# Performance work log

Hardware: AMD Instinct MI355X
Metric: run time of the kernel (lower is better)

Reference implementation:

```python
import jax, jax.numpy as jnp
import numpy as np

C = 3            # image_channels
X = 192          # cortex_x_count
Y = 192          # cortex_y_count
RF = 24          # receptive field height/width
IMG = 224        # input image H/W (must be >= max rf_start + RF)
EXK = 38         # excitatory lateral window (i-19:i+19)
INK = 94         # inhibitory lateral window (i-47:i+47)
PAD = 47         # activation padding used by the original module
GAMMA_E = 0.9
GAMMA_I = 0.9


def setup_inputs() -> dict:
    key = jax.random.key(0)
    ks = jax.random.split(key, 9)
    return {
        "input": jax.random.normal(ks[0], (C, IMG, IMG), jnp.float32),
        "afferent_weights": jax.random.normal(ks[1], (C, X, Y, RF, RF), jnp.float32),
        "ex_lateral_weight": jax.random.normal(ks[2], (EXK, EXK), jnp.float32),
        "in_lateral_weight": jax.random.normal(ks[3], (INK, INK), jnp.float32),
        "afferent_mask": jax.random.uniform(ks[4], (RF, RF), jnp.float32),
        "ex_lateral_mask": jax.random.uniform(ks[5], (EXK, EXK), jnp.float32),
        "in_lateral_mask": jax.random.uniform(ks[6], (INK, INK), jnp.float32),
        "old_activation": jax.random.normal(ks[7], (C, X, Y), jnp.float32),
        "cortex_rf_start": jax.random.randint(ks[8], (X, Y, 2), 0, IMG - RF + 1, jnp.int32),
    }


def _lateral(old_pad, kernel2d, out_start):
    # Depthwise correlation: same 2D kernel applied to every channel.
    # old_pad: (C, X+2*PAD, Y+2*PAD); treat channels as batch.
    y = jax.lax.conv_general_dilated(
        old_pad[:, None],              # (C, 1, Hp, Wp)
        kernel2d[None, None],          # (1, 1, K, K)
        window_strides=(1, 1),
        padding="VALID",
    )[:, 0]                            # (C, Ho, Wo)
    return y[:, out_start:out_start + X, out_start:out_start + Y]


def reference(input, afferent_weights, ex_lateral_weight, in_lateral_weight,
              afferent_mask, ex_lateral_mask, in_lateral_mask,
              old_activation, cortex_rf_start):
    # --- afferent: per-pixel locally-connected receptive fields ---
    u = jnp.arange(RF)
    ix = cortex_rf_start[..., 0][:, :, None, None] + u[None, None, :, None]  # (X,Y,RF,1)
    iy = cortex_rf_start[..., 1][:, :, None, None] + u[None, None, None, :]  # (X,Y,1,RF)
    patches = input[:, ix, iy]                                               # (C,X,Y,RF,RF)
    afferent = jnp.einsum("cxyuv,cxyuv->xy", patches,
                          afferent_weights * afferent_mask)                  # (X,Y)

    # --- lateral fields over padded previous activation ---
    old_pad = jnp.pad(old_activation, ((0, 0), (PAD, PAD), (PAD, PAD)))
    # excitatory window [i-19:i+19] centered at cell (i+47) -> start offset 28
    exc = _lateral(old_pad, ex_lateral_weight * ex_lateral_mask, PAD - 19)
    # inhibitory window [i-47:i+47] -> start offset 0
    inh = _lateral(old_pad, in_lateral_weight * in_lateral_mask, PAD - 47)

    # afferent sum is a scalar per cortex location, shared across channels
    return jnp.broadcast_to(afferent[None], (C, X, Y)) + GAMMA_E * exc - GAMMA_I * inh
```

## Files before the change

### kernel.cpp

```cpp
#include <hip/hip_runtime.h>

#define XD 192
#define YD 192
#define CCH 3
#define IMG 224

#define OFF_PAD 0
#define PADW 320
#define N_PAD (CCH*XD*PADW)
#define OFF_KI (OFF_PAD + N_PAD)
#define KI_LD 96
#define N_KI (94*KI_LD)
#define OFF_KE (OFF_KI + N_KI)
#define KE_LD 40
#define N_KE (38*KE_LD)

#define N_OUT (CCH*XD*YD)

#define QSPLIT 8
#define NCONV 576
#define NAFF 9216

typedef __attribute__((ext_vector_type(4))) float f32x4;

__global__ __launch_bounds__(256) void k_prep(
    const float* __restrict__ exw, const float* __restrict__ exm,
    const float* __restrict__ inw, const float* __restrict__ inm,
    const float* __restrict__ oldact, float* __restrict__ ws,
    float* __restrict__ out)
{
    const int TOT = N_OUT + N_PAD + N_KI + N_KE;
    for (int idx = blockIdx.x * 256 + threadIdx.x; idx < TOT; idx += gridDim.x * 256) {
        if (idx < N_OUT) {
            out[idx] = 0.f;
        } else if (idx < N_OUT + N_PAD) {
            const int k = idx - N_OUT;
            const int col = k % PADW;
            const int rem = k / PADW;
            float v = 0.f;
            if (col >= 64 && col < 64 + YD)
                v = oldact[rem * YD + (col - 64)];
            ws[OFF_PAD + k] = v;
        } else if (idx < N_OUT + N_PAD + N_KI) {
            const int k = idx - N_OUT - N_PAD;
            const int i = k / KI_LD, j = k % KI_LD;
            ws[OFF_KI + k] = (j < 94) ? (-0.9f * inw[i * 94 + j] * inm[i * 94 + j]) : 0.f;
        } else {
            const int k = idx - N_OUT - N_PAD - N_KI;
            const int i = k / KE_LD, j = k % KE_LD;
            ws[OFF_KE + k] = (j < 38) ? (0.9f * exw[i * 38 + j] * exm[i * 38 + j]) : 0.f;
        }
    }
}

__global__ __launch_bounds__(256, 3) void k_fused(
    const float* __restrict__ input, const float* __restrict__ affw,
    const float* __restrict__ affm, const int* __restrict__ rfstart,
    const float* __restrict__ ws, float* __restrict__ out)
{
    const int bid = blockIdx.x;
    const int tid = threadIdx.x;

    if (bid < NCONV) {
        const int xt = bid % 24;
        const int c  = (bid / 24) % 3;
        const int q  = bid / 72;
        const int yg = tid & 31;
        const int xr = tid >> 5;
        const int x  = xt * 8 + xr;
        const int y0 = yg * 6;

        float acc[6] = {0.f, 0.f, 0.f, 0.f, 0.f, 0.f};
        const float* pad = ws + OFF_PAD + (size_t)c * XD * PADW;

        for (int i = q; i < 94; i += QSPLIT) {
            const int r = x + i - 47;
            if (r < 0 || r >= XD) continue;
            const float* row = pad + r * PADW + y0 + 17;
            const float4* kw = (const float4*)(ws + OFF_KI + i * KI_LD);
            float w[9];
            #pragma unroll
            for (int k = 0; k < 9; ++k) w[k] = row[k];
            #pragma unroll
            for (int g = 0; g < 24; ++g) {
                const float4 k4 = kw[g];
                #pragma unroll
                for (int t = 0; t < 6; ++t) {
                    acc[t] += k4.x * w[0 + t];
                    acc[t] += k4.y * w[1 + t];
                    acc[t] += k4.z * w[2 + t];
                    acc[t] += k4.w * w[3 + t];
                }
                #pragma unroll
                for (int k = 0; k < 5; ++k) w[k] = w[k + 4];
                #pragma unroll
                for (int k = 5; k < 9; ++k) w[k] = row[4 * (g + 1) + k];
            }
        }

        for (int i = q; i < 38; i += QSPLIT) {
            const int r = x + i - 19;
            if (r < 0 || r >= XD) continue;
            const float* row = pad + r * PADW + y0 + 45;
            const float4* kw = (const float4*)(ws + OFF_KE + i * KE_LD);
            float w[9];
            #pragma unroll
            for (int k = 0; k < 9; ++k) w[k] = row[k];
            #pragma unroll
            for (int g = 0; g < 10; ++g) {
                const float4 k4 = kw[g];
                #pragma unroll
                for (int t = 0; t < 6; ++t) {
                    acc[t] += k4.x * w[0 + t];
                    acc[t] += k4.y * w[1 + t];
                    acc[t] += k4.z * w[2 + t];
                    acc[t] += k4.w * w[3 + t];
                }
                #pragma unroll
                for (int k = 0; k < 5; ++k) w[k] = w[k + 4];
                #pragma unroll
                for (int k = 5; k < 9; ++k) w[k] = row[4 * (g + 1) + k];
            }
        }

        float* op = out + ((size_t)c * XD + x) * YD + y0;
        #pragma unroll
        for (int t = 0; t < 6; ++t) atomicAdd(&op[t], acc[t]);

    } else {
        const int wv_id = __builtin_amdgcn_readfirstlane(tid >> 6);
        const int xy    = (bid - NCONV) * 4 + wv_id;
        const int lane  = tid & 63;
        const int sx = rfstart[xy * 2 + 0];
        const int sy = rfstart[xy * 2 + 1];
        const f32x4* W4 = (const f32x4*)affw + (size_t)xy * 144;
        const f32x4* M4 = (const f32x4*)affm;

        f32x4 wv[7], mv[7], iv[7];

        #pragma unroll
        for (int it = 0; it < 7; ++it) {
            const int g0 = lane + (it << 6);
            const int g  = (g0 < 432) ? g0 : 0;
            const int c  = (g >= 288) ? 2 : ((g >= 144) ? 1 : 0);
            const int r  = g - c * 144;
            const f32x4* wp = W4 + (size_t)c * 5308416 + r;
            asm volatile("global_load_dwordx4 %0, %1, off"
                         : "=v"(wv[it]) : "v"(wp));
            const int u  = (r * 2731) >> 14;
            const int v  = (r - u * 6) << 2;
            const float* ip = input + c * (IMG * IMG) + (sx + u) * IMG + (sy + v);
            asm volatile("global_load_dwordx4 %0, %1, off"
                         : "=v"(iv[it]) : "v"(ip));
            const f32x4* mp = M4 + r;
            asm volatile("global_load_dwordx4 %0, %1, off"
                         : "=v"(mv[it]) : "v"(mp));
        }
        asm volatile("s_waitcnt vmcnt(0)" ::: "memory");
        __builtin_amdgcn_sched_barrier(0);

        float acc = 0.f;
        #pragma unroll
        for (int it = 0; it < 7; ++it) {
            const int g0 = lane + (it << 6);
            const float z = (g0 < 432) ? 1.f : 0.f;
            acc += iv[it].x * (z * mv[it].x) * wv[it].x;
            acc += iv[it].y * (z * mv[it].y) * wv[it].y;
            acc += iv[it].z * (z * mv[it].z) * wv[it].z;
            acc += iv[it].w * (z * mv[it].w) * wv[it].w;
        }
        #pragma unroll
        for (int off = 32; off > 0; off >>= 1) acc += __shfl_xor(acc, off);
        if (lane < 3) atomicAdd(out + (size_t)lane * (XD * YD) + xy, acc);
    }
}

extern "C" void kernel_launch(void* const* d_in, const int* in_sizes, int n_in,
                              void* d_out, int out_size, void* d_ws, size_t ws_size,
                              hipStream_t stream)
{
    const float* input   = (const float*)d_in[0];
    const float* affw    = (const float*)d_in[1];
    const float* exw     = (const float*)d_in[2];
    const float* inw     = (const float*)d_in[3];
    const float* affm    = (const float*)d_in[4];
    const float* exm     = (const float*)d_in[5];
    const float* inm     = (const float*)d_in[6];
    const float* oldact  = (const float*)d_in[7];
    const int*   rfstart = (const int*)d_in[8];
    float* out = (float*)d_out;
    float* ws  = (float*)d_ws;

    hipLaunchKernelGGL(k_prep, dim3(1194), dim3(256), 0, stream,
                       exw, exm, inw, inm, oldact, ws, out);

    hipLaunchKernelGGL(k_fused, dim3(NCONV + NAFF), dim3(256), 0, stream,
                       input, affw, affm, rfstart, ws, out);
}
```

Measured before the change: 95.36 us.

## Stage lateral activation rows in LDS and widen per-thread output tile

```diff
diff --git a/kernel.cpp b/kernel.cpp
--- a/kernel.cpp
+++ b/kernel.cpp
@@ -5,8 +5,8 @@
 #define CCH 3
 #define IMG 224
 
+#define PADW 288
 #define OFF_PAD 0
-#define PADW 320
 #define N_PAD (CCH*XD*PADW)
 #define OFF_KI (OFF_PAD + N_PAD)
 #define KI_LD 96
@@ -17,8 +17,8 @@
 
 #define N_OUT (CCH*XD*YD)
 
-#define QSPLIT 8
-#define NCONV 576
+#define QS 16
+#define NCONV (12*3*QS)
 #define NAFF 9216
 
 typedef __attribute__((ext_vector_type(4))) float f32x4;
@@ -35,11 +35,11 @@
             out[idx] = 0.f;
         } else if (idx < N_OUT + N_PAD) {
             const int k = idx - N_OUT;
-            const int col = k % PADW;
+            const int t = k % PADW;
             const int rem = k / PADW;
             float v = 0.f;
-            if (col >= 64 && col < 64 + YD)
-                v = oldact[rem * YD + (col - 64)];
+            if (t >= 47 && t < 47 + YD)
+                v = oldact[rem * YD + (t - 47)];
             ws[OFF_PAD + k] = v;
         } else if (idx < N_OUT + N_PAD + N_KI) {
             const int k = idx - N_OUT - N_PAD;
@@ -58,74 +58,107 @@
     const float* __restrict__ affm, const int* __restrict__ rfstart,
     const float* __restrict__ ws, float* __restrict__ out)
 {
+    __shared__ float s_act[16][PADW];
+
     const int bid = blockIdx.x;
     const int tid = threadIdx.x;
 
     if (bid < NCONV) {
-        const int xt = bid % 24;
-        const int c  = (bid / 24) % 3;
-        const int q  = bid / 72;
-        const int yg = tid & 31;
-        const int xr = tid >> 5;
-        const int x  = xt * 8 + xr;
-        const int y0 = yg * 6;
-
-        float acc[6] = {0.f, 0.f, 0.f, 0.f, 0.f, 0.f};
-        const float* pad = ws + OFF_PAD + (size_t)c * XD * PADW;
-
-        for (int i = q; i < 94; i += QSPLIT) {
-            const int r = x + i - 47;
-            if (r < 0 || r >= XD) continue;
-            const float* row = pad + r * PADW + y0 + 17;
+        const int slab = bid % 12;
+        const int c    = (bid / 12) % 3;
+        const int q    = bid / 36;
+        const int x0   = slab * 16;
+        const int xr   = tid >> 4;
+        const int yg   = tid & 15;
+        const int y0   = yg * 12;
+
+        const float* wspad_c = ws + OFF_PAD + (size_t)c * XD * PADW;
+
+        float acc[12];
+        #pragma unroll
+        for (int t = 0; t < 12; ++t) acc[t] = 0.f;
+
+        for (int i = q; i < 94; i += QS) {
+            const int r0 = x0 + i - 47;
+            if (r0 > XD - 1 || r0 < -15) continue;
+            __syncthreads();
+            for (int p = tid; p < 16 * 72; p += 256) {
+                const int row = p / 72;
+                const int c4  = (p - row * 72) * 4;
+                const int rr  = r0 + row;
+                float4 v = {0.f, 0.f, 0.f, 0.f};
+                if ((unsigned)rr < XD)
+                    v = *(const float4*)(wspad_c + rr * PADW + c4);
+                *(float4*)(&s_act[row][c4]) = v;
+            }
+            __syncthreads();
+
+            const float* arow = s_act[xr] + y0;
             const float4* kw = (const float4*)(ws + OFF_KI + i * KI_LD);
-            float w[9];
-            #pragma unroll
-            for (int k = 0; k < 9; ++k) w[k] = row[k];
+            float w[16];
+            #pragma unroll
+            for (int k = 0; k < 4; ++k)
+                *(float4*)&w[4 * k] = *(const float4*)(arow + 4 * k);
             #pragma unroll
             for (int g = 0; g < 24; ++g) {
                 const float4 k4 = kw[g];
                 #pragma unroll
-                for (int t = 0; t < 6; ++t) {
-                    acc[t] += k4.x * w[0 + t];
-                    acc[t] += k4.y * w[1 + t];
-                    acc[t] += k4.z * w[2 + t];
-                    acc[t] += k4.w * w[3 + t];
-                }
-                #pragma unroll
-                for (int k = 0; k < 5; ++k) w[k] = w[k + 4];
-                #pragma unroll
-                for (int k = 5; k < 9; ++k) w[k] = row[4 * (g + 1) + k];
-            }
-        }
-
-        for (int i = q; i < 38; i += QSPLIT) {
-            const int r = x + i - 19;
-            if (r < 0 || r >= XD) continue;
-            const float* row = pad + r * PADW + y0 + 45;
+                for (int t = 0; t < 12; ++t) {
+                    acc[t] += k4.x * w[t + 0];
+                    acc[t] += k4.y * w[t + 1];
+                    acc[t] += k4.z * w[t + 2];
+                    acc[t] += k4.w * w[t + 3];
+                }
+                if (g < 23) {
+                    #pragma unroll
+                    for (int k = 0; k < 12; ++k) w[k] = w[k + 4];
+                    *(float4*)&w[12] = *(const float4*)(arow + 4 * g + 16);
+                }
+            }
+        }
+
+        for (int i = q; i < 38; i += QS) {
+            const int r0 = x0 + i - 19;
+            if (r0 > XD - 1 || r0 < -15) continue;
+            __syncthreads();
+            for (int p = tid; p < 16 * 72; p += 256) {
+                const int row = p / 72;
+                const int c4  = (p - row * 72) * 4;
+                const int rr  = r0 + row;
+                float4 v = {0.f, 0.f, 0.f, 0.f};
+                if ((unsigned)rr < XD)
+                    v = *(const float4*)(wspad_c + rr * PADW + c4);
+                *(float4*)(&s_act[row][c4]) = v;
+            }
+            __syncthreads();
+
+            const float* arow = s_act[xr] + y0 + 28;
             const float4* kw = (const float4*)(ws + OFF_KE + i * KE_LD);
-            float w[9];
-            #pragma unroll
-            for (int k = 0; k < 9; ++k) w[k] = row[k];
+            float w[16];
+            #pragma unroll
+            for (int k = 0; k < 4; ++k)
+                *(float4*)&w[4 * k] = *(const float4*)(arow + 4 * k);
             #pragma unroll
             for (int g = 0; g < 10; ++g) {
                 const float4 k4 = kw[g];
                 #pragma unroll
-                for (int t = 0; t < 6; ++t) {
-                    acc[t] += k4.x * w[0 + t];
-                    acc[t] += k4.y * w[1 + t];
-                    acc[t] += k4.z * w[2 + t];
-                    acc[t] += k4.w * w[3 + t];
-                }
-                #pragma unroll
-                for (int k = 0; k < 5; ++k) w[k] = w[k + 4];
-                #pragma unroll
-                for (int k = 5; k < 9; ++k) w[k] = row[4 * (g + 1) + k];
-            }
-        }
-
-        float* op = out + ((size_t)c * XD + x) * YD + y0;
-        #pragma unroll
-        for (int t = 0; t < 6; ++t) atomicAdd(&op[t], acc[t]);
+                for (int t = 0; t < 12; ++t) {
+                    acc[t] += k4.x * w[t + 0];
+                    acc[t] += k4.y * w[t + 1];
+                    acc[t] += k4.z * w[t + 2];
+                    acc[t] += k4.w * w[t + 3];
+                }
+                if (g < 9) {
+                    #pragma unroll
+                    for (int k = 0; k < 12; ++k) w[k] = w[k + 4];
+                    *(float4*)&w[12] = *(const float4*)(arow + 4 * g + 16);
+                }
+            }
+        }
+
+        float* op = out + ((size_t)c * XD + (x0 + xr)) * YD + y0;
+        #pragma unroll
+        for (int t = 0; t < 12; ++t) atomicAdd(&op[t], acc[t]);
 
     } else {
         const int wv_id = __builtin_amdgcn_readfirstlane(tid >> 6);
@@ -191,7 +224,7 @@
     float* out = (float*)d_out;
     float* ws  = (float*)d_ws;
 
-    hipLaunchKernelGGL(k_prep, dim3(1194), dim3(256), 0, stream,
+    hipLaunchKernelGGL(k_prep, dim3(1122), dim3(256), 0, stream,
                        exw, exm, inw, inm, oldact, ws, out);
 
     hipLaunchKernelGGL(k_fused, dim3(NCONV + NAFF), dim3(256), 0, stream,
```

Measured after the change: 126.7 us. 32.9% more time.

## Restructure lateral conv: one wave per row staged in LDS, fused exc/inh passes

Applied to the files above, without the earlier changes.

```diff
diff --git a/kernel.cpp b/kernel.cpp
--- a/kernel.cpp
+++ b/kernel.cpp
@@ -5,8 +5,8 @@
 #define CCH 3
 #define IMG 224
 
+#define PADW 288
 #define OFF_PAD 0
-#define PADW 320
 #define N_PAD (CCH*XD*PADW)
 #define OFF_KI (OFF_PAD + N_PAD)
 #define KI_LD 96
@@ -17,8 +17,8 @@
 
 #define N_OUT (CCH*XD*YD)
 
-#define QSPLIT 8
-#define NCONV 576
+#define QS 4
+#define NCONV (144*QS)
 #define NAFF 9216
 
 typedef __attribute__((ext_vector_type(4))) float f32x4;
@@ -35,11 +35,11 @@
             out[idx] = 0.f;
         } else if (idx < N_OUT + N_PAD) {
             const int k = idx - N_OUT;
-            const int col = k % PADW;
+            const int t = k % PADW;
             const int rem = k / PADW;
             float v = 0.f;
-            if (col >= 64 && col < 64 + YD)
-                v = oldact[rem * YD + (col - 64)];
+            if (t >= 47 && t < 47 + YD)
+                v = oldact[rem * YD + (t - 47)];
             ws[OFF_PAD + k] = v;
         } else if (idx < N_OUT + N_PAD + N_KI) {
             const int k = idx - N_OUT - N_PAD;
@@ -58,74 +58,85 @@
     const float* __restrict__ affm, const int* __restrict__ rfstart,
     const float* __restrict__ ws, float* __restrict__ out)
 {
+    __shared__ float s_row[4][PADW];
+
     const int bid = blockIdx.x;
     const int tid = threadIdx.x;
 
     if (bid < NCONV) {
-        const int xt = bid % 24;
-        const int c  = (bid / 24) % 3;
-        const int q  = bid / 72;
-        const int yg = tid & 31;
-        const int xr = tid >> 5;
-        const int x  = xt * 8 + xr;
-        const int y0 = yg * 6;
-
-        float acc[6] = {0.f, 0.f, 0.f, 0.f, 0.f, 0.f};
-        const float* pad = ws + OFF_PAD + (size_t)c * XD * PADW;
-
-        for (int i = q; i < 94; i += QSPLIT) {
+        const int grp  = bid >> 2;
+        const int q    = bid & 3;
+        const int w    = tid >> 6;
+        const int lane = tid & 63;
+        const int rowid = grp * 4 + w;
+        const int c = rowid / XD;
+        const int x = rowid - c * XD;
+
+        float* srow = &s_row[w][0];
+        const float* padc = ws + OFF_PAD + (size_t)(c * XD) * PADW;
+        const int bix = 3 * lane;
+
+        float acc0 = 0.f, acc1 = 0.f, acc2 = 0.f;
+
+        for (int i = q; i < 94; i += QS) {
             const int r = x + i - 47;
-            if (r < 0 || r >= XD) continue;
-            const float* row = pad + r * PADW + y0 + 17;
-            const float4* kw = (const float4*)(ws + OFF_KI + i * KI_LD);
-            float w[9];
-            #pragma unroll
-            for (int k = 0; k < 9; ++k) w[k] = row[k];
-            #pragma unroll
-            for (int g = 0; g < 24; ++g) {
-                const float4 k4 = kw[g];
+            if ((unsigned)r >= (unsigned)XD) continue;
+
+            const float* src = padc + r * PADW;
+            *(float4*)(srow + 4 * lane) = *(const float4*)(src + 4 * lane);
+            if (lane < 8)
+                *(float4*)(srow + 256 + 4 * lane) =
+                    *(const float4*)(src + 256 + 4 * lane);
+
+            {
+                const float* ki = ws + OFF_KI + i * KI_LD;
+                float a0 = srow[bix + 0], a1 = srow[bix + 1], a2 = srow[bix + 2];
+                float a3 = srow[bix + 3], a4 = srow[bix + 4];
                 #pragma unroll
-                for (int t = 0; t < 6; ++t) {
-                    acc[t] += k4.x * w[0 + t];
-                    acc[t] += k4.y * w[1 + t];
-                    acc[t] += k4.z * w[2 + t];
-                    acc[t] += k4.w * w[3 + t];
+                for (int g = 0; g < 31; ++g) {
+                    const float k0 = ki[3 * g + 0];
+                    const float k1 = ki[3 * g + 1];
+                    const float k2 = ki[3 * g + 2];
+                    acc0 += k0 * a0 + k1 * a1 + k2 * a2;
+                    acc1 += k0 * a1 + k1 * a2 + k2 * a3;
+                    acc2 += k0 * a2 + k1 * a3 + k2 * a4;
+                    a0 = a3; a1 = a4;
+                    a2 = srow[bix + 3 * g + 5];
+                    a3 = srow[bix + 3 * g + 6];
+                    a4 = srow[bix + 3 * g + 7];
                 }
+                const float k93 = ki[93];
+                acc0 += k93 * a0; acc1 += k93 * a1; acc2 += k93 * a2;
+            }
+
+            if ((unsigned)(i - 28) < 38u) {
+                const float* ke = ws + OFF_KE + (i - 28) * KE_LD;
+                float b0 = srow[bix + 28], b1 = srow[bix + 29], b2 = srow[bix + 30];
+                float b3 = srow[bix + 31], b4 = srow[bix + 32];
                 #pragma unroll
-                for (int k = 0; k < 5; ++k) w[k] = w[k + 4];
-                #pragma unroll
-                for (int k = 5; k < 9; ++k) w[k] = row[4 * (g + 1) + k];
+                for (int g = 0; g < 12; ++g) {
+                    const float k0 = ke[3 * g + 0];
+                    const float k1 = ke[3 * g + 1];
+                    const float k2 = ke[3 * g + 2];
+                    acc0 += k0 * b0 + k1 * b1 + k2 * b2;
+                    acc1 += k0 * b1 + k1 * b2 + k2 * b3;
+                    acc2 += k0 * b2 + k1 * b3 + k2 * b4;
+                    b0 = b3; b1 = b4;
+                    b2 = srow[bix + 28 + 3 * g + 5];
+                    b3 = srow[bix + 28 + 3 * g + 6];
+                    b4 = srow[bix + 28 + 3 * g + 7];
+                }
+                const float k36 = ke[36], k37 = ke[37];
+                acc0 += k36 * b0 + k37 * b1;
+                acc1 += k36 * b1 + k37 * b2;
+                acc2 += k36 * b2 + k37 * b3;
             }
         }
 
-        for (int i = q; i < 38; i += QSPLIT) {
-            const int r = x + i - 19;
-            if (r < 0 || r >= XD) continue;
-            const float* row = pad + r * PADW + y0 + 45;
-            const float4* kw = (const float4*)(ws + OFF_KE + i * KE_LD);
-            float w[9];
-            #pragma unroll
-            for (int k = 0; k < 9; ++k) w[k] = row[k];
-            #pragma unroll
-            for (int g = 0; g < 10; ++g) {
-                const float4 k4 = kw[g];
-                #pragma unroll
-                for (int t = 0; t < 6; ++t) {
-                    acc[t] += k4.x * w[0 + t];
-                    acc[t] += k4.y * w[1 + t];
-                    acc[t] += k4.z * w[2 + t];
-                    acc[t] += k4.w * w[3 + t];
-                }
-                #pragma unroll
-                for (int k = 0; k < 5; ++k) w[k] = w[k + 4];
-                #pragma unroll
-                for (int k = 5; k < 9; ++k) w[k] = row[4 * (g + 1) + k];
-            }
-        }
-
-        float* op = out + ((size_t)c * XD + x) * YD + y0;
-        #pragma unroll
-        for (int t = 0; t < 6; ++t) atomicAdd(&op[t], acc[t]);
+        float* op = out + ((size_t)c * XD + x) * YD + 3 * lane;
+        atomicAdd(op + 0, acc0);
+        atomicAdd(op + 1, acc1);
+        atomicAdd(op + 2, acc2);
 
     } else {
         const int wv_id = __builtin_amdgcn_readfirstlane(tid >> 6);
@@ -191,7 +202,7 @@
     float* out = (float*)d_out;
     float* ws  = (float*)d_ws;
 
-    hipLaunchKernelGGL(k_prep, dim3(1194), dim3(256), 0, stream,
+    hipLaunchKernelGGL(k_prep, dim3(1122), dim3(256), 0, stream,
                        exw, exm, inw, inm, oldact, ws, out);
 
     hipLaunchKernelGGL(k_fused, dim3(NCONV + NAFF), dim3(256), 0, stream,
```

New measurement: 80.41 us. 15.7% less time.
